# Kernel optimization log

Measured on AMD Instinct MI355X. Metric: run time of the kernel, lower is better.

## Reference

```python
import jax, jax.numpy as jnp
import numpy as np

N, T, H, W, C = 64, 32, 64, 64, 256
HID, NB, P, OUT = 512, 12, 7, 388
CIN = P * P + 2  # 49 patch values + 2 normalized coords


def _ln(x, s):
    # haiku LayerNorm(axis=-1, create_scale=True, create_offset=False), eps=1e-5
    m = jnp.mean(x, axis=-1, keepdims=True)
    v = jnp.var(x, axis=-1, keepdims=True)
    return (x - m) * jax.lax.rsqrt(v + 1e-5) * s


def _dwconv(x, w, b, groups):
    # hk.DepthwiseConv1D, NWC, stride 1, SAME padding; w: [K, 1, C_out]
    y = jax.lax.conv_general_dilated(
        x, w, (1,), 'SAME', dimension_numbers=('NWC', 'WIO', 'NWC'),
        feature_group_count=groups)
    return y + b


def _forward(feature_grid, query_feats, pos, in_w, in_b, dw1_w, dw1_b, dw2_w,
             dw2_b, ln1_s, ln2_s, up_w, up_b, down_w, down_b, lnf_s, out_w,
             out_b):
    pad = P - 1
    # cost volume: einsum('bnc,bthwc->tbnhw') with batch=1, laid out [N,T,H,W]
    corrs = jnp.einsum('nc,thwc->nthw', query_feats, feature_grid)
    padded = jnp.pad(corrs, ((0, 0), (0, 0), (pad, pad), (pad, pad)))
    # extract_patch_depthwise_conv: the separable bilinear bump kernel convolved
    # VALID over the padded map equals a bilinear sample at (o + pos + P/2 - 1).
    pp = pos + P / 2.0 - 1.0  # [N,T,2] (y,x)
    iy = jnp.floor(pp[..., 0])
    ix = jnp.floor(pp[..., 1])
    fy = (pp[..., 0] - iy)[..., None, None]
    fx = (pp[..., 1] - ix)[..., None, None]
    offs = jnp.arange(P, dtype=jnp.int32)
    y0 = iy.astype(jnp.int32)[..., None] + offs  # [N,T,P]
    x0 = ix.astype(jnp.int32)[..., None] + offs  # [N,T,P]
    gat = jax.vmap(jax.vmap(lambda img, yi, xi: img[yi][:, xi]))
    patch = ((1 - fy) * (1 - fx) * gat(padded, y0, x0)
             + (1 - fy) * fx * gat(padded, y0, x0 + 1)
             + fy * (1 - fx) * gat(padded, y0 + 1, x0)
             + fy * fx * gat(padded, y0 + 1, x0 + 1))  # [N,T,P,P]
    x = jnp.concatenate(
        [patch.reshape(patch.shape[0], patch.shape[1], P * P),
         pos / jnp.float32(H)], axis=-1)  # [N,T,CIN]
    # PIPSMLPMixer
    x = x @ in_w + in_b  # [N,T,HID]
    for i in range(NB):
        # PIPsConvBlock: depthwise_conv_residual
        skip = x
        h = _ln(x, ln1_s[i])
        h = jax.nn.gelu(_dwconv(h, dw1_w[i], dw1_b[i], HID))  # ch mult 4
        h = _dwconv(h, dw2_w[i], dw2_b[i], HID * 4)           # ch mult 1
        h = h[..., 0::4] + h[..., 1::4] + h[..., 2::4] + h[..., 3::4]
        x = h + skip
        # conv_channels_mixer
        skip = x
        h = _ln(x, ln2_s[i])
        h = jax.nn.gelu(h @ up_w[i] + up_b[i]) @ down_w[i] + down_b[i]
        x = h + skip
    x = _ln(x, lnf_s)
    return x @ out_w + out_b  # [N,T,OUT]


def setup_inputs() -> dict:
    key = jax.random.key(0)
    ks = jax.random.split(key, 12)
    s = 0.02
    return dict(
        feature_grid=jax.random.normal(ks[0], (T, H, W, C), jnp.float32),
        query_feats=jax.random.normal(ks[1], (N, C), jnp.float32),
        pos=jax.random.uniform(ks[2], (N, T, 2), jnp.float32) * (H - 8),
        in_w=jax.random.normal(ks[3], (CIN, HID), jnp.float32) * s,
        in_b=jnp.zeros((HID,), jnp.float32),
        dw1_w=jax.random.normal(ks[4], (NB, 3, 1, HID * 4), jnp.float32) * s,
        dw1_b=jnp.zeros((NB, HID * 4), jnp.float32),
        dw2_w=jax.random.normal(ks[5], (NB, 3, 1, HID * 4), jnp.float32) * s,
        dw2_b=jnp.zeros((NB, HID * 4), jnp.float32),
        ln1_s=jnp.ones((NB, HID), jnp.float32),
        ln2_s=jnp.ones((NB, HID), jnp.float32),
        up_w=jax.random.normal(ks[6], (NB, HID, HID * 4), jnp.float32) * s,
        up_b=jnp.zeros((NB, HID * 4), jnp.float32),
        down_w=jax.random.normal(ks[7], (NB, HID * 4, HID), jnp.float32) * s,
        down_b=jnp.zeros((NB, HID), jnp.float32),
        lnf_s=jnp.ones((HID,), jnp.float32),
        out_w=jax.random.normal(ks[8], (HID, OUT), jnp.float32) * s,
        out_b=jnp.zeros((OUT,), jnp.float32),
    )


def reference(feature_grid, query_feats, pos, in_w, in_b, dw1_w, dw1_b, dw2_w,
              dw2_b, ln1_s, ln2_s, up_w, up_b, down_w, down_b, lnf_s, out_w,
              out_b):
    return _forward(feature_grid, query_feats, pos, in_w, in_b, dw1_w, dw1_b,
                    dw2_w, dw2_b, ln1_s, ln2_s, up_w, up_b, down_w, down_b,
                    lnf_s, out_w, out_b)
```

## Files before the change

kernel.cpp:

```cpp
#include <hip/hip_runtime.h>
#include <hip/hip_bf16.h>

#define N_    64
#define T_    32
#define H_    64
#define W_    64
#define C_    256
#define HID   512
#define HID4  2048
#define NBLK  12
#define P_    7
#define OUT_  388
#define OUTP  448
#define CIN   51
#define M_    (N_*T_)

typedef __attribute__((ext_vector_type(4))) float f32x4;
typedef __attribute__((ext_vector_type(8))) short bf16x8;

__device__ __forceinline__ float gelu_f(float x) {
    float x3 = x * x * x;
    return 0.5f * x * (1.f + tanhf(0.7978845608028654f * (x + 0.044715f * x3)));
}

__device__ __forceinline__ void gload_lds16(const void* g, void* l) {
    __builtin_amdgcn_global_load_lds(
        (const __attribute__((address_space(1))) void*)g,
        (__attribute__((address_space(3))) void*)l, 16, 0, 0);
}

__global__ __launch_bounds__(256) void pre_kernel(
    const float* __restrict__ fg, const float* __restrict__ qf,
    const float* __restrict__ pos, const float* __restrict__ in_w,
    const float* __restrict__ in_b, float* __restrict__ x,
    const float* __restrict__ up_w, const float* __restrict__ dn_w,
    const float* __restrict__ out_w, __hip_bfloat16* __restrict__ upT,
    __hip_bfloat16* __restrict__ dnT, __hip_bfloat16* __restrict__ outT) {
    __shared__ float4 q[64];
    __shared__ float g[8][8];
    __shared__ float xrow[CIN];
    __shared__ float tile[32][33];
    int bid = blockIdx.x;
    int tid = threadIdx.x;

    if (bid < M_) {
        int m = bid;
        int n = m >> 5;
        int t = m & (T_ - 1);
        int wid = tid >> 6, lane = tid & 63;
        if (tid < 64) q[tid] = *(const float4*)&qf[n * C_ + tid * 4];
        __syncthreads();
        float posy = pos[m * 2 + 0];
        float posx = pos[m * 2 + 1];
        float py = posy + 2.5f;
        float px = posx + 2.5f;
        int iy = (int)floorf(py), ix = (int)floorf(px);
        float fy = py - (float)iy, fx = px - (float)ix;
        float4 qv = q[lane];
        #pragma unroll
        for (int i = 0; i < 16; ++i) {
            int idx = wid * 16 + i;
            int a = idx >> 3, b = idx & 7;
            int y = iy + a - 6, xc = ix + b - 6;
            float partial = 0.f;
            if (y >= 0 && y < H_ && xc >= 0 && xc < W_) {
                const float4* fp = (const float4*)&fg[(((t * H_ + y) * W_) + xc) * C_];
                float4 v = fp[lane];
                partial = v.x * qv.x + v.y * qv.y + v.z * qv.z + v.w * qv.w;
            }
            #pragma unroll
            for (int o2 = 32; o2; o2 >>= 1) partial += __shfl_xor(partial, o2);
            if (lane == 0) g[a][b] = partial;
        }
        __syncthreads();
        if (tid < 49) {
            int p = tid / 7, qq = tid % 7;
            xrow[tid] = (1.f - fy) * (1.f - fx) * g[p][qq]
                      + (1.f - fy) * fx         * g[p][qq + 1]
                      + fy         * (1.f - fx) * g[p + 1][qq]
                      + fy         * fx         * g[p + 1][qq + 1];
        } else if (tid == 49) {
            xrow[49] = posy * (1.f / 64.f);
        } else if (tid == 50) {
            xrow[50] = posx * (1.f / 64.f);
        }
        __syncthreads();
        float acc0 = in_b[tid], acc1 = in_b[tid + 256];
        #pragma unroll
        for (int c = 0; c < CIN; ++c) {
            float rv = xrow[c];
            acc0 += rv * in_w[c * HID + tid];
            acc1 += rv * in_w[c * HID + tid + 256];
        }
        x[m * HID + tid] = acc0;
        x[m * HID + tid + 256] = acc1;
        return;
    }

    bid -= M_;
    const float* src;
    __hip_bfloat16* dst;
    int R, C, bx, by;
    if (bid < 12288) {
        int z = bid >> 10, r = bid & 1023;
        src = up_w + (size_t)z * HID * HID4;
        dst = upT + (size_t)z * HID4 * HID;
        R = HID; C = HID4; bx = r & 63; by = r >> 6;
    } else if (bid < 24576) {
        bid -= 12288;
        int z = bid >> 10, r = bid & 1023;
        src = dn_w + (size_t)z * HID4 * HID;
        dst = dnT + (size_t)z * HID * HID4;
        R = HID4; C = HID; bx = r & 15; by = r >> 4;
    } else {
        bid -= 24576;
        src = out_w; dst = outT;
        R = HID; C = OUT_; bx = bid % 14; by = bid / 14;
    }
    int c0 = bx * 32, r0 = by * 32;
    int tx = tid & 31, ty = tid >> 5;
    #pragma unroll
    for (int i = 0; i < 4; ++i) {
        int r = r0 + ty + i * 8, c = c0 + tx;
        tile[ty + i * 8][tx] = (c < C) ? src[(size_t)r * C + c] : 0.f;
    }
    __syncthreads();
    #pragma unroll
    for (int i = 0; i < 4; ++i) {
        int c = c0 + ty + i * 8, r = r0 + tx;
        dst[(size_t)c * R + r] = __float2bfloat16(tile[tx][ty + i * 8]);
    }
}

__global__ __launch_bounds__(512) void fused_dw_kernel(
    const float* __restrict__ xin, float* __restrict__ xout,
    __hip_bfloat16* __restrict__ t1T,
    const float* __restrict__ ln1s, const float* __restrict__ ln2s,
    const float* __restrict__ w1, const float* __restrict__ b1,
    const float* __restrict__ w2, const float* __restrict__ b2) {
    __shared__ float2 part[12][8];
    int n = blockIdx.y;
    int t0 = blockIdx.x * 8;
    int j = threadIdx.x;
    int lane = j & 63, wave = j >> 6;

    float xv[12];
    #pragma unroll
    for (int tt = 0; tt < 12; ++tt) {
        int t = t0 - 2 + tt;
        xv[tt] = (t >= 0 && t < T_) ? xin[(n * T_ + t) * HID + j] : 0.f;
    }
    #pragma unroll
    for (int tt = 0; tt < 12; ++tt) {
        float s = xv[tt], q = xv[tt] * xv[tt];
        #pragma unroll
        for (int o = 32; o; o >>= 1) { s += __shfl_xor(s, o); q += __shfl_xor(q, o); }
        if (lane == 0) part[tt][wave] = make_float2(s, q);
    }
    __syncthreads();
    float s1v = ln1s[j];
    float xl[12];
    #pragma unroll
    for (int tt = 0; tt < 12; ++tt) {
        int t = t0 - 2 + tt;
        if (t >= 0 && t < T_) {
            float s = 0.f, q = 0.f;
            #pragma unroll
            for (int w = 0; w < 8; ++w) { float2 p = part[tt][w]; s += p.x; q += p.y; }
            float mean = s * (1.f / HID);
            float var  = q * (1.f / HID) - mean * mean;
            xl[tt] = (xv[tt] - mean) * rsqrtf(var + 1e-5f) * s1v;
        } else xl[tt] = 0.f;
    }
    float w1a[12], w2a[12], b1a[4];
    #pragma unroll
    for (int r = 0; r < 3; ++r) {
        *(float4*)&w1a[r * 4] = *(const float4*)&w1[r * HID4 + 4 * j];
        *(float4*)&w2a[r * 4] = *(const float4*)&w2[r * HID4 + 4 * j];
    }
    *(float4*)&b1a[0] = *(const float4*)&b1[4 * j];
    float4 b2v = *(const float4*)&b2[4 * j];
    float h[8];
    float b2sum = b2v.x + b2v.y + b2v.z + b2v.w;
    #pragma unroll
    for (int i = 0; i < 8; ++i) h[i] = b2sum;
    #pragma unroll
    for (int k = 0; k < 4; ++k) {
        float gk[10];
        #pragma unroll
        for (int idx = 0; idx < 10; ++idx) {
            int tp = t0 - 1 + idx;
            if (tp >= 0 && tp < T_) {
                float a = b1a[k] + w1a[0 * 4 + k] * xl[idx]
                                 + w1a[1 * 4 + k] * xl[idx + 1]
                                 + w1a[2 * 4 + k] * xl[idx + 2];
                gk[idx] = gelu_f(a);
            } else gk[idx] = 0.f;
        }
        #pragma unroll
        for (int i = 0; i < 8; ++i)
            h[i] += w2a[0 * 4 + k] * gk[i] + w2a[1 * 4 + k] * gk[i + 1]
                  + w2a[2 * 4 + k] * gk[i + 2];
    }
    float xn[8];
    #pragma unroll
    for (int i = 0; i < 8; ++i) xn[i] = xv[i + 2] + h[i];
    __syncthreads();
    #pragma unroll
    for (int i = 0; i < 8; ++i) {
        float s = xn[i], q = xn[i] * xn[i];
        #pragma unroll
        for (int o = 32; o; o >>= 1) { s += __shfl_xor(s, o); q += __shfl_xor(q, o); }
        if (lane == 0) part[i][wave] = make_float2(s, q);
    }
    __syncthreads();
    float s2v = ln2s[j];
    int cbase = j >> 3, csub = j & 7;
    #pragma unroll
    for (int i = 0; i < 8; ++i) {
        float s = 0.f, q = 0.f;
        #pragma unroll
        for (int w = 0; w < 8; ++w) { float2 p = part[i][w]; s += p.x; q += p.y; }
        float mean = s * (1.f / HID);
        float var  = q * (1.f / HID) - mean * mean;
        float rstd = rsqrtf(var + 1e-5f);
        int row = n * T_ + t0 + i;
        xout[row * HID + j] = xn[i];
        t1T[((size_t)cbase * M_ + row) * 8 + csub] =
            __float2bfloat16((xn[i] - mean) * rstd * s2v);
    }
}

__global__ __launch_bounds__(256) void ln_kernel(
    const float* __restrict__ in, const float* __restrict__ s,
    __hip_bfloat16* __restrict__ t1T) {
    int wid = threadIdx.x >> 6, lane = threadIdx.x & 63;
    int row = blockIdx.x * 4 + wid;
    const float* r = in + row * HID + lane * 8;
    float4 v0 = *(const float4*)r;
    float4 v1 = *(const float4*)(r + 4);
    float sum = v0.x + v0.y + v0.z + v0.w + v1.x + v1.y + v1.z + v1.w;
    float sq  = v0.x*v0.x + v0.y*v0.y + v0.z*v0.z + v0.w*v0.w
              + v1.x*v1.x + v1.y*v1.y + v1.z*v1.z + v1.w*v1.w;
    #pragma unroll
    for (int o = 32; o; o >>= 1) { sum += __shfl_xor(sum, o); sq += __shfl_xor(sq, o); }
    float mean = sum * (1.f / HID);
    float var  = sq * (1.f / HID) - mean * mean;
    float rstd = rsqrtf(var + 1e-5f);
    const float* sp = s + lane * 8;
    float4 s0 = *(const float4*)sp;
    float4 s1 = *(const float4*)(sp + 4);
    float o[8];
    o[0] = (v0.x - mean) * rstd * s0.x; o[1] = (v0.y - mean) * rstd * s0.y;
    o[2] = (v0.z - mean) * rstd * s0.z; o[3] = (v0.w - mean) * rstd * s0.w;
    o[4] = (v1.x - mean) * rstd * s1.x; o[5] = (v1.y - mean) * rstd * s1.y;
    o[6] = (v1.z - mean) * rstd * s1.z; o[7] = (v1.w - mean) * rstd * s1.w;
    alignas(16) __hip_bfloat16 tmp[8];
    #pragma unroll
    for (int i = 0; i < 8; ++i) tmp[i] = __float2bfloat16(o[i]);
    *(bf16x8*)&t1T[((size_t)lane * M_ + row) * 8] = *(bf16x8*)tmp;
}

template <int EPI, int SWZ, int NT>
__global__ __launch_bounds__(256, 4) void gemm_regA(
    const __hip_bfloat16* __restrict__ At,
    const __hip_bfloat16* __restrict__ Bt,
    const float* __restrict__ bias, float* __restrict__ Cf,
    __hip_bfloat16* __restrict__ Cb, int ldN, int Nstore) {
    constexpr int K = 512;
    __shared__ alignas(16) __hip_bfloat16 Bs[2][64 * 64];
    int tid = threadIdx.x;
    int lane = tid & 63, w = tid >> 6;

    int row0, col0base;
    if (SWZ) {
        int bid = blockIdx.y * gridDim.x + blockIdx.x;
        int xcd = bid & 7;
        int i = bid >> 3;
        row0 = (xcd * 4 + (i & 3)) * 64;
        col0base = (i >> 2) * (64 * NT);
    } else {
        row0 = blockIdx.y * 64;
        col0base = blockIdx.x * (64 * NT);
    }

    int sub = lane >> 4;
    int arow = row0 + w * 16 + (lane & 15);
    bf16x8 areg[16];
    #pragma unroll
    for (int kb = 0; kb < 16; ++kb) {
        int c = kb * 4 + sub;
        areg[kb] = *(const bf16x8*)&At[((size_t)c * M_ + arow) * 8];
    }

    int rI = lane >> 3;
    int cp = lane & 7;
    auto stageB = [&](int buf, int k0, int col0) {
        #pragma unroll
        for (int s = 0; s < 2; ++s) {
            int rbase = w * 16 + s * 8;
            int row = rbase + rI;
            int corig = cp ^ (row & 7);
            gload_lds16(Bt + (size_t)(col0 + row) * K + k0 + corig * 8,
                        (char*)Bs[buf] + rbase * 128);
        }
    };

    int cr = (lane >> 4) * 4;
    int cc = lane & 15;

    #pragma unroll 1
    for (int t = 0; t < NT; ++t) {
        int col0 = col0base + t * 64;
        f32x4 acc[4];
        #pragma unroll
        for (int n = 0; n < 4; ++n) acc[n] = (f32x4){0.f, 0.f, 0.f, 0.f};

        stageB(0, 0, col0);
        #pragma unroll
        for (int step = 0; step < 8; ++step) {
            int cur = step & 1;
            __builtin_amdgcn_s_barrier();
            if (step < 7) {
                stageB(cur ^ 1, (step + 1) * 64, col0);
                asm volatile("s_waitcnt vmcnt(2)" ::: "memory");
            } else {
                asm volatile("s_waitcnt vmcnt(0)" ::: "memory");
            }
            __builtin_amdgcn_sched_barrier(0);
            __builtin_amdgcn_s_barrier();
            __builtin_amdgcn_sched_barrier(0);
            #pragma unroll
            for (int kk = 0; kk < 2; ++kk) {
                bf16x8 bfr[4];
                #pragma unroll
                for (int n = 0; n < 4; ++n) {
                    int row = n * 16 + (lane & 15);
                    int chunk = (kk * 4 + sub) ^ (row & 7);
                    bfr[n] = *(const bf16x8*)((const char*)Bs[cur] + row * 128 + chunk * 16);
                }
                __builtin_amdgcn_s_setprio(1);
                #pragma unroll
                for (int n = 0; n < 4; ++n)
                    acc[n] = __builtin_amdgcn_mfma_f32_16x16x32_bf16(
                        areg[step * 2 + kk], bfr[n], acc[n], 0, 0, 0);
                __builtin_amdgcn_s_setprio(0);
            }
        }

        #pragma unroll
        for (int n = 0; n < 4; ++n) {
            #pragma unroll
            for (int j = 0; j < 4; ++j) {
                int row = row0 + w * 16 + cr + j;
                int col = col0 + n * 16 + cc;
                float v = acc[n][j];
                if (EPI == 0) {
                    if (col < Nstore)
                        Cf[(size_t)row * Nstore + col] = v + bias[col];
                } else {
                    v = gelu_f(v + bias[col]);
                    Cb[(size_t)row * ldN + col] = __float2bfloat16(v);
                }
            }
        }
    }
}

__global__ __launch_bounds__(512) void gemm_down(
    const __hip_bfloat16* __restrict__ A, const __hip_bfloat16* __restrict__ Bt,
    const float* __restrict__ bias, float* __restrict__ Cf,
    int K, int ldN) {
    __shared__ alignas(16) __hip_bfloat16 As[2][2][64 * 64];
    __shared__ alignas(16) __hip_bfloat16 Bs[2][2][64 * 64];
    int tid = threadIdx.x;
    int lane = tid & 63, wave = tid >> 6;
    int g = wave >> 2;
    int w4 = wave & 3;
    int wr = w4 >> 1, wc = w4 & 1;

    int bid = blockIdx.y * gridDim.x + blockIdx.x;
    int xcd = bid & 7;
    int i = bid >> 3;
    int row0 = (xcd * 4 + (i & 3)) * 64;
    int col0 = (i >> 2) * 64;

    int Kg = K / 2;
    int kbase = g * Kg;

    f32x4 acc[2][2];
    #pragma unroll
    for (int m = 0; m < 2; ++m)
        #pragma unroll
        for (int n = 0; n < 2; ++n)
            acc[m][n] = (f32x4){0.f, 0.f, 0.f, 0.f};

    int rI = lane >> 3;
    int cp = lane & 7;

    auto stage = [&](int buf, int k0) {
        #pragma unroll
        for (int s = 0; s < 2; ++s) {
            int rbase = w4 * 16 + s * 8;
            int row = rbase + rI;
            int corig = cp ^ (row & 7);
            gload_lds16(A + (size_t)(row0 + row) * K + kbase + k0 + corig * 8,
                        (char*)As[g][buf] + rbase * 128);
        }
        #pragma unroll
        for (int s = 0; s < 2; ++s) {
            int rbase = w4 * 16 + s * 8;
            int row = rbase + rI;
            int corig = cp ^ (row & 7);
            gload_lds16(Bt + (size_t)(col0 + row) * K + kbase + k0 + corig * 8,
                        (char*)Bs[g][buf] + rbase * 128);
        }
    };

    int nsteps = Kg >> 6;
    stage(0, 0);
    for (int step = 0; step < nsteps; ++step) {
        int cur = step & 1;
        __builtin_amdgcn_s_barrier();
        if (step + 1 < nsteps) {
            stage(cur ^ 1, (step + 1) * 64);
            asm volatile("s_waitcnt vmcnt(4)" ::: "memory");
        } else {
            asm volatile("s_waitcnt vmcnt(0)" ::: "memory");
        }
        __builtin_amdgcn_sched_barrier(0);
        __builtin_amdgcn_s_barrier();
        __builtin_amdgcn_sched_barrier(0);
        #pragma unroll
        for (int kk = 0; kk < 2; ++kk) {
            bf16x8 af[2], bfr[2];
            #pragma unroll
            for (int m = 0; m < 2; ++m) {
                int row = wr * 32 + m * 16 + (lane & 15);
                int chunk2 = (kk * 4 + (lane >> 4)) ^ (row & 7);
                af[m] = *(const bf16x8*)((const char*)As[g][cur] + row * 128 + chunk2 * 16);
            }
            #pragma unroll
            for (int n = 0; n < 2; ++n) {
                int row = wc * 32 + n * 16 + (lane & 15);
                int chunk2 = (kk * 4 + (lane >> 4)) ^ (row & 7);
                bfr[n] = *(const bf16x8*)((const char*)Bs[g][cur] + row * 128 + chunk2 * 16);
            }
            __builtin_amdgcn_s_setprio(1);
            #pragma unroll
            for (int m = 0; m < 2; ++m)
                #pragma unroll
                for (int n = 0; n < 2; ++n)
                    acc[m][n] = __builtin_amdgcn_mfma_f32_16x16x32_bf16(
                        af[m], bfr[n], acc[m][n], 0, 0, 0);
            __builtin_amdgcn_s_setprio(0);
        }
    }

    int cr = (lane >> 4) * 4;
    int cc = lane & 15;

    float* scratch = (float*)&As[0][0][0];
    __syncthreads();
    if (g == 1) {
        #pragma unroll
        for (int m = 0; m < 2; ++m)
            #pragma unroll
            for (int n = 0; n < 2; ++n)
                #pragma unroll
                for (int j = 0; j < 4; ++j)
                    scratch[(wr * 32 + m * 16 + cr + j) * 64 +
                            wc * 32 + n * 16 + cc] = acc[m][n][j];
    }
    __syncthreads();
    if (g == 1) return;
    #pragma unroll
    for (int m = 0; m < 2; ++m) {
        #pragma unroll
        for (int n = 0; n < 2; ++n) {
            #pragma unroll
            for (int j = 0; j < 4; ++j) {
                int row = row0 + wr * 32 + m * 16 + cr + j;
                int col = col0 + wc * 32 + n * 16 + cc;
                float v = acc[m][n][j] +
                          scratch[(wr * 32 + m * 16 + cr + j) * 64 +
                                  wc * 32 + n * 16 + cc];
                Cf[(size_t)row * ldN + col] += v + bias[col];
            }
        }
    }
}

extern "C" void kernel_launch(void* const* d_in, const int* in_sizes, int n_in,
                              void* d_out, int out_size, void* d_ws, size_t ws_size,
                              hipStream_t stream) {
    const float* fg     = (const float*)d_in[0];
    const float* qf     = (const float*)d_in[1];
    const float* pos    = (const float*)d_in[2];
    const float* in_w   = (const float*)d_in[3];
    const float* in_b   = (const float*)d_in[4];
    const float* dw1_w  = (const float*)d_in[5];
    const float* dw1_b  = (const float*)d_in[6];
    const float* dw2_w  = (const float*)d_in[7];
    const float* dw2_b  = (const float*)d_in[8];
    const float* ln1_s  = (const float*)d_in[9];
    const float* ln2_s  = (const float*)d_in[10];
    const float* up_w   = (const float*)d_in[11];
    const float* up_b   = (const float*)d_in[12];
    const float* down_w = (const float*)d_in[13];
    const float* down_b = (const float*)d_in[14];
    const float* lnf_s  = (const float*)d_in[15];
    const float* out_w  = (const float*)d_in[16];
    const float* out_b  = (const float*)d_in[17];
    float* out = (float*)d_out;

    char* ws = (char*)d_ws;
    float* xa = (float*)ws;                        ws += (size_t)M_ * HID * 4;
    float* xb = (float*)ws;                        ws += (size_t)M_ * HID * 4;
    __hip_bfloat16* t1T = (__hip_bfloat16*)ws;     ws += (size_t)M_ * HID * 2;
    __hip_bfloat16* t2b = (__hip_bfloat16*)ws;     ws += (size_t)M_ * HID4 * 2;
    __hip_bfloat16* upT  = (__hip_bfloat16*)ws;    ws += (size_t)NBLK * HID4 * HID * 2;
    __hip_bfloat16* dnT  = (__hip_bfloat16*)ws;    ws += (size_t)NBLK * HID * HID4 * 2;
    __hip_bfloat16* outT = (__hip_bfloat16*)ws;    ws += (size_t)OUTP * HID * 2;

    pre_kernel<<<26848, 256, 0, stream>>>(
        fg, qf, pos, in_w, in_b, xa, up_w, down_w, out_w, upT, dnT, outT);

    float* xc = xa;
    float* xn = xb;
    for (int b = 0; b < NBLK; ++b) {
        fused_dw_kernel<<<dim3(4, N_), 512, 0, stream>>>(
            xc, xn, t1T, ln1_s + b * HID, ln2_s + b * HID,
            dw1_w + b * 3 * HID4, dw1_b + b * HID4,
            dw2_w + b * 3 * HID4, dw2_b + b * HID4);
        gemm_regA<1, 1, 2><<<dim3(HID4 / 128, M_ / 64), 256, 0, stream>>>(
            t1T, upT + (size_t)b * HID4 * HID, up_b + b * HID4, nullptr, t2b,
            HID4, HID4);
        gemm_down<<<dim3(HID / 64, M_ / 64), 512, 0, stream>>>(
            t2b, dnT + (size_t)b * HID * HID4, down_b + b * HID, xn,
            HID4, HID);
        float* tmp = xc; xc = xn; xn = tmp;
    }

    ln_kernel<<<M_ / 4, 256, 0, stream>>>(xc, lnf_s, t1T);
    gemm_regA<0, 0, 1><<<dim3(OUTP / 64, M_ / 64), 256, 0, stream>>>(
        t1T, outT, out_b, out, nullptr, OUT_, OUT_);
}
```

Baseline: 625.1 us.

## Rework cost-volume patch dot products and weight transpose to use wider loads

The correlation patch computation now has 16 lanes cooperate on each dot product, each loading 16 floats in four float4 reads. A wave therefore handles four patch positions per iteration with a shorter shuffle reduction, and the shared-memory query staging and its barrier are gone. The weight transpose-to-bf16 path drops the shared-memory tile and instead has each thread gather 8 strided k values and write one 16-byte bf16x8 vector. Each block covers a 64x64 tile, cutting the block count from 26848 to 8248. The trade-off is strided, only partially coalesced global reads in the transpose, traded for fewer blocks and wider stores.

```diff
diff --git a/kernel.cpp b/kernel.cpp
--- a/kernel.cpp
+++ b/kernel.cpp
@@ -29,6 +29,10 @@
         (__attribute__((address_space(3))) void*)l, 16, 0, 0);
 }
 
+__device__ __forceinline__ float dot4(float4 a, float4 b) {
+    return a.x * b.x + a.y * b.y + a.z * b.z + a.w * b.w;
+}
+
 __global__ __launch_bounds__(256) void pre_kernel(
     const float* __restrict__ fg, const float* __restrict__ qf,
     const float* __restrict__ pos, const float* __restrict__ in_w,
@@ -36,10 +40,8 @@
     const float* __restrict__ up_w, const float* __restrict__ dn_w,
     const float* __restrict__ out_w, __hip_bfloat16* __restrict__ upT,
     __hip_bfloat16* __restrict__ dnT, __hip_bfloat16* __restrict__ outT) {
-    __shared__ float4 q[64];
-    __shared__ float g[8][8];
-    __shared__ float xrow[CIN];
-    __shared__ float tile[32][33];
+    __shared__ float gsm[8][8];
+    __shared__ float xrow[CIN + 1];
     int bid = blockIdx.x;
     int tid = threadIdx.x;
 
@@ -48,37 +50,46 @@
         int n = m >> 5;
         int t = m & (T_ - 1);
         int wid = tid >> 6, lane = tid & 63;
-        if (tid < 64) q[tid] = *(const float4*)&qf[n * C_ + tid * 4];
-        __syncthreads();
+        int g = lane >> 4, p16 = lane & 15;
         float posy = pos[m * 2 + 0];
         float posx = pos[m * 2 + 1];
         float py = posy + 2.5f;
         float px = posx + 2.5f;
         int iy = (int)floorf(py), ix = (int)floorf(px);
         float fy = py - (float)iy, fx = px - (float)ix;
-        float4 qv = q[lane];
-        #pragma unroll
-        for (int i = 0; i < 16; ++i) {
-            int idx = wid * 16 + i;
+        const float* qp = &qf[n * C_ + p16 * 16];
+        float4 qv0 = *(const float4*)(qp + 0);
+        float4 qv1 = *(const float4*)(qp + 4);
+        float4 qv2 = *(const float4*)(qp + 8);
+        float4 qv3 = *(const float4*)(qp + 12);
+        #pragma unroll
+        for (int outer = 0; outer < 4; ++outer) {
+            int idx = wid * 16 + outer * 4 + g;
             int a = idx >> 3, b = idx & 7;
             int y = iy + a - 6, xc = ix + b - 6;
             float partial = 0.f;
             if (y >= 0 && y < H_ && xc >= 0 && xc < W_) {
-                const float4* fp = (const float4*)&fg[(((t * H_ + y) * W_) + xc) * C_];
-                float4 v = fp[lane];
-                partial = v.x * qv.x + v.y * qv.y + v.z * qv.z + v.w * qv.w;
-            }
-            #pragma unroll
-            for (int o2 = 32; o2; o2 >>= 1) partial += __shfl_xor(partial, o2);
-            if (lane == 0) g[a][b] = partial;
+                const float* fp = &fg[(((t * H_ + y) * W_) + xc) * C_ + p16 * 16];
+                float4 v0 = *(const float4*)(fp + 0);
+                float4 v1 = *(const float4*)(fp + 4);
+                float4 v2 = *(const float4*)(fp + 8);
+                float4 v3 = *(const float4*)(fp + 12);
+                partial = dot4(v0, qv0) + dot4(v1, qv1)
+                        + dot4(v2, qv2) + dot4(v3, qv3);
+            }
+            partial += __shfl_xor(partial, 1);
+            partial += __shfl_xor(partial, 2);
+            partial += __shfl_xor(partial, 4);
+            partial += __shfl_xor(partial, 8);
+            if (p16 == 0) gsm[a][b] = partial;
         }
         __syncthreads();
         if (tid < 49) {
             int p = tid / 7, qq = tid % 7;
-            xrow[tid] = (1.f - fy) * (1.f - fx) * g[p][qq]
-                      + (1.f - fy) * fx         * g[p][qq + 1]
-                      + fy         * (1.f - fx) * g[p + 1][qq]
-                      + fy         * fx         * g[p + 1][qq + 1];
+            xrow[tid] = (1.f - fy) * (1.f - fx) * gsm[p][qq]
+                      + (1.f - fy) * fx         * gsm[p][qq + 1]
+                      + fy         * (1.f - fx) * gsm[p + 1][qq]
+                      + fy         * fx         * gsm[p + 1][qq + 1];
         } else if (tid == 49) {
             xrow[49] = posy * (1.f / 64.f);
         } else if (tid == 50) {
@@ -100,35 +111,41 @@
     bid -= M_;
     const float* src;
     __hip_bfloat16* dst;
-    int R, C, bx, by;
-    if (bid < 12288) {
-        int z = bid >> 10, r = bid & 1023;
+    int Kd, Cn, nt, kt;
+    if (bid < 3072) {
+        int z = bid >> 8, r = bid & 255;
         src = up_w + (size_t)z * HID * HID4;
         dst = upT + (size_t)z * HID4 * HID;
-        R = HID; C = HID4; bx = r & 63; by = r >> 6;
-    } else if (bid < 24576) {
-        bid -= 12288;
-        int z = bid >> 10, r = bid & 1023;
+        Kd = HID; Cn = HID4;
+        nt = r & 31; kt = r >> 5;
+    } else if (bid < 6144) {
+        bid -= 3072;
+        int z = bid >> 8, r = bid & 255;
         src = dn_w + (size_t)z * HID4 * HID;
         dst = dnT + (size_t)z * HID * HID4;
-        R = HID4; C = HID; bx = r & 15; by = r >> 4;
+        Kd = HID4; Cn = HID;
+        nt = r & 7; kt = r >> 3;
     } else {
-        bid -= 24576;
+        bid -= 6144;
         src = out_w; dst = outT;
-        R = HID; C = OUT_; bx = bid % 14; by = bid / 14;
-    }
-    int c0 = bx * 32, r0 = by * 32;
-    int tx = tid & 31, ty = tid >> 5;
-    #pragma unroll
-    for (int i = 0; i < 4; ++i) {
-        int r = r0 + ty + i * 8, c = c0 + tx;
-        tile[ty + i * 8][tx] = (c < C) ? src[(size_t)r * C + c] : 0.f;
-    }
-    __syncthreads();
-    #pragma unroll
-    for (int i = 0; i < 4; ++i) {
-        int c = c0 + ty + i * 8, r = r0 + tx;
-        dst[(size_t)c * R + r] = __float2bfloat16(tile[tx][ty + i * 8]);
+        Kd = HID; Cn = OUT_;
+        nt = bid % 7; kt = bid / 7;
+    }
+    int lane = tid & 63, w = tid >> 6;
+    int n = nt * 64 + lane;
+    int k0 = kt * 64 + w * 16;
+    bool inb = (n < Cn);
+    #pragma unroll
+    for (int oct = 0; oct < 2; ++oct) {
+        int kb = k0 + oct * 8;
+        float v[8];
+        #pragma unroll
+        for (int i = 0; i < 8; ++i)
+            v[i] = inb ? src[(size_t)(kb + i) * Cn + n] : 0.f;
+        alignas(16) __hip_bfloat16 h[8];
+        #pragma unroll
+        for (int i = 0; i < 8; ++i) h[i] = __float2bfloat16(v[i]);
+        *(bf16x8*)&dst[(size_t)n * Kd + kb] = *(bf16x8*)h;
     }
 }
 
@@ -523,7 +540,7 @@
     __hip_bfloat16* dnT  = (__hip_bfloat16*)ws;    ws += (size_t)NBLK * HID * HID4 * 2;
     __hip_bfloat16* outT = (__hip_bfloat16*)ws;    ws += (size_t)OUTP * HID * 2;
 
-    pre_kernel<<<26848, 256, 0, stream>>>(
+    pre_kernel<<<8248, 256, 0, stream>>>(
         fg, qf, pos, in_w, in_b, xa, up_w, down_w, out_w, upT, dnT, outT);
 
     float* xc = xa;
```

New measurement: 645.5 us. 1.03x slower.
